# Optimization experiments

Measured on AMD Instinct MI355X. Metric: run time of the kernel, lower is better.

Reference implementation:

```python
import jax, jax.numpy as jnp
import numpy as np

N_HEADS = 12


def gconv1x1(x, w, b, groups):
    # x: [B, C, T, S]; w: [O, C//groups] (1x1 kernel squeezed); b: [O]
    B, C, T, S = x.shape
    O, I = w.shape
    xr = x.reshape(B, groups, C // groups, T, S)
    wr = w.reshape(groups, O // groups, I)
    y = jnp.einsum('bgits,goi->bgots', xr, wr).reshape(B, O, T, S)
    return y + b[None, :, None, None]


def setup_inputs() -> dict:
    key = jax.random.key(0)
    ks = jax.random.split(key, 16)
    B, T, E = 2, 512, 768
    H = N_HEADS
    s = 0.02
    inp = {
        'x': jax.random.normal(ks[0], (B, T, E), jnp.float32),
        # fc_q / fc_k / fc_v (torch Linear: y = x @ W.T + b)
        'wq': jax.random.normal(ks[1], (E, E), jnp.float32) * s,
        'bq': jax.random.normal(ks[2], (E,), jnp.float32) * s,
        'wk': jax.random.normal(ks[3], (E, E), jnp.float32) * s,
        'bk': jax.random.normal(ks[4], (E,), jnp.float32) * s,
        'wv': jax.random.normal(ks[5], (E, E), jnp.float32) * s,
        'bv': jax.random.normal(ks[6], (E,), jnp.float32) * s,
        # ConvolutionOp: all 1x1 grouped convs, groups=12
        # conv_inner_subspace_1: in=144 -> out=96  (w: [96, 12])
        'w1': jax.random.normal(ks[7], (8 * H, H), jnp.float32) * s,
        'b1': jax.random.normal(ks[8], (8 * H,), jnp.float32) * s,
        # conv_inner_subspace_2: in=96 -> out=12   (w: [12, 8])
        'w2': jax.random.normal(ks[9], (H, 8), jnp.float32) * s,
        'b2': jax.random.normal(ks[10], (H,), jnp.float32) * s,
        # conv_cross_subspace_1: in=12 -> out=48   (w: [48, 1])
        'w3': jax.random.normal(ks[11], (4 * H, 1), jnp.float32) * s,
        'b3': jax.random.normal(ks[12], (4 * H,), jnp.float32) * s,
        # conv_cross_subspace_2: in=48 -> out=12   (w: [12, 4])
        'w4': jax.random.normal(ks[13], (H, 4), jnp.float32) * s,
        'b4': jax.random.normal(ks[14], (H,), jnp.float32) * s,
    }
    return inp


def reference(x, wq, bq, wk, bk, wv, bv, w1, b1, w2, b2, w3, b3, w4, b4):
    B, T, E = x.shape
    H = N_HEADS
    hd = E // H
    scale = E ** 0.5  # note: sqrt(embed_dim), not sqrt(head_dim)

    def heads(y):  # [B,T,E] -> [H,B,T,hd]
        return y.reshape(B, T, H, hd).transpose(2, 0, 1, 3)

    q = heads(x @ wq.T + bq)
    k = heads(x @ wk.T + bk)
    v = heads(x @ wv.T + bv)

    # all head-pair QK^T: channel index = q_head * H + k_head (matches torch stack order)
    attn = jnp.einsum('qbld,kbtd->qkblt', q, k) / scale          # [H,H,B,T,T]
    attn = attn.transpose(2, 0, 1, 3, 4).reshape(B, H * H, T, T)  # [B,144,T,T]

    # talking-heads style grouped 1x1 conv mixing
    a = jax.nn.relu(gconv1x1(attn, w1, b1, H))   # [B,96,T,T]
    a = gconv1x1(a, w2, b2, H)                    # [B,12,T,T]
    a = jax.nn.relu(gconv1x1(a, w3, b3, H))      # [B,48,T,T]
    a = gconv1x1(a, w4, b4, H)                    # [B,12,T,T]

    # weighted V sum; rearrange 'head b t d -> b t (head d)'
    ctx = jnp.einsum('bhlt,hbtd->blhd', a, v).reshape(B, T, E)
    return ctx
```

## Files before the change

### kernel.cpp

```cpp
#include <hip/hip_runtime.h>

#define DEVINL __device__ __forceinline__

constexpr int E    = 768;
constexpr int TSEQ = 512;
constexpr int NH   = 12;
constexpr int HD   = 64;
constexpr float RSCALE = 0.036084391824351615f;

typedef short bf16x8 __attribute__((ext_vector_type(8)));
typedef float floatx4 __attribute__((ext_vector_type(4)));

DEVINL short f2bf(float x) {
    union { float f; unsigned u; } v; v.f = x;
    unsigned r = v.u + 0x7FFFu + ((v.u >> 16) & 1u);
    return (short)(r >> 16);
}
DEVINL float bf2f(short s) {
    union { unsigned u; float f; } v;
    v.u = ((unsigned)(unsigned short)s) << 16;
    return v.f;
}

__global__ __launch_bounds__(256) void convert_kernel(
    const float* __restrict__ x,  const float* __restrict__ wq,
    const float* __restrict__ wk, const float* __restrict__ wv,
    short* __restrict__ xb, short* __restrict__ wqb,
    short* __restrict__ wkb, short* __restrict__ wvb)
{
    const int g = blockIdx.x * 256 + threadIdx.x;
    const float* src; short* dst; int off;
    if (g < 98304)       { src = x;  dst = xb;  off = g * 8; }
    else if (g < 172032) { src = wq; dst = wqb; off = (g - 98304) * 8; }
    else if (g < 245760) { src = wk; dst = wkb; off = (g - 172032) * 8; }
    else                 { src = wv; dst = wvb; off = (g - 245760) * 8; }
    float4 f0 = *(const float4*)&src[off];
    float4 f1 = *(const float4*)&src[off + 4];
    bf16x8 o;
    o[0] = f2bf(f0.x); o[1] = f2bf(f0.y); o[2] = f2bf(f0.z); o[3] = f2bf(f0.w);
    o[4] = f2bf(f1.x); o[5] = f2bf(f1.y); o[6] = f2bf(f1.z); o[7] = f2bf(f1.w);
    *(bf16x8*)&dst[off] = o;
}

__global__ __launch_bounds__(256) void qkv_mfma(
    const short* __restrict__ xb,
    const short* __restrict__ wqb, const float* __restrict__ bq,
    const short* __restrict__ wkb, const float* __restrict__ bk,
    const short* __restrict__ wvb, const float* __restrict__ bv,
    short* __restrict__ Qo, short* __restrict__ Ko, short* __restrict__ Vo)
{
    const short* W; const float* bias; short* outp;
    if (blockIdx.z == 0)      { W = wqb; bias = bq; outp = Qo; }
    else if (blockIdx.z == 1) { W = wkb; bias = bk; outp = Ko; }
    else                      { W = wvb; bias = bv; outp = Vo; }

    __shared__ short As[64 * 72];
    __shared__ short Bs[64 * 72];

    const int m0   = blockIdx.x * 64;
    const int n0   = blockIdx.y * 64;
    const int tid  = threadIdx.x;
    const int wvi  = tid >> 6;
    const int lane = tid & 63;
    const int col  = lane & 15;
    const int quad = lane >> 4;

    const int r0 = tid >> 3,   kc0 = tid & 7;
    const int r1 = r0 + 32;

    floatx4 acc[4];
    #pragma unroll
    for (int i = 0; i < 4; i++) acc[i] = (floatx4){0.f, 0.f, 0.f, 0.f};

    for (int k0 = 0; k0 < E; k0 += 64) {
        bf16x8 a0 = *(const bf16x8*)&xb[(size_t)(m0 + r0) * E + k0 + kc0 * 8];
        bf16x8 a1 = *(const bf16x8*)&xb[(size_t)(m0 + r1) * E + k0 + kc0 * 8];
        bf16x8 b0 = *(const bf16x8*)&W [(size_t)(n0 + r0) * E + k0 + kc0 * 8];
        bf16x8 b1 = *(const bf16x8*)&W [(size_t)(n0 + r1) * E + k0 + kc0 * 8];
        __syncthreads();
        *(bf16x8*)&As[r0 * 72 + kc0 * 8] = a0;
        *(bf16x8*)&As[r1 * 72 + kc0 * 8] = a1;
        *(bf16x8*)&Bs[r0 * 72 + kc0 * 8] = b0;
        *(bf16x8*)&Bs[r1 * 72 + kc0 * 8] = b1;
        __syncthreads();
        #pragma unroll
        for (int k32 = 0; k32 < 2; k32++) {
            bf16x8 bf = *(const bf16x8*)&Bs[(wvi*16 + col) * 72 + k32*32 + quad*8];
            #pragma unroll
            for (int ms = 0; ms < 4; ms++) {
                bf16x8 af = *(const bf16x8*)&As[(ms*16 + col) * 72 + k32*32 + quad*8];
                acc[ms] = __builtin_amdgcn_mfma_f32_16x16x32_bf16(af, bf, acc[ms], 0, 0, 0);
            }
        }
    }

    const float bn = bias[n0 + wvi*16 + col];
    const int h = blockIdx.y;
    #pragma unroll
    for (int ms = 0; ms < 4; ms++) {
        #pragma unroll
        for (int r = 0; r < 4; r++) {
            int m = m0 + ms*16 + quad*4 + r;
            int bb = m >> 9, l = m & 511;
            outp[(((size_t)(bb*NH + h)) * TSEQ + l) * HD + wvi*16 + col] =
                f2bf(acc[ms][r] + bn);
        }
    }
}

__global__ __launch_bounds__(256) void kmix_kernel(
    const short* __restrict__ K,
    const float* __restrict__ w1,
    short* __restrict__ Kp)
{
    const int g  = blockIdx.x * 256 + threadIdx.x;
    const int d8 = g & 7;
    const int t  = (g >> 3) & 511;
    const int o  = (g >> 12) & 7;
    const int bh = g >> 15;
    const int h  = bh % NH;
    const int b  = bh / NH;

    float acc[8] = {};
    #pragma unroll
    for (int i = 0; i < 12; i++) {
        float w = w1[(h*8 + o)*12 + i] * RSCALE;
        bf16x8 kv = *(const bf16x8*)&K[(((size_t)(b*NH + i) * TSEQ) + t) * HD + d8*8];
        #pragma unroll
        for (int j = 0; j < 8; j++)
            acc[j] = fmaf(w, bf2f(kv[j]), acc[j]);
    }
    bf16x8 outv;
    #pragma unroll
    for (int j = 0; j < 8; j++) outv[j] = f2bf(acc[j]);
    *(bf16x8*)&Kp[(size_t)g * 8] = outv;
}

DEVINL float mlp_eval(const float s[8],
                      const float b1r[8], const float w2r[8], float b2r,
                      const float w3r[4], const float b3r[4],
                      const float w4r[4], float b4r)
{
    float z2 = b2r;
    #pragma unroll
    for (int o = 0; o < 8; o++) {
        float z1 = fmaxf(s[o] + b1r[o], 0.0f);
        z2 = fmaf(z1, w2r[o], z2);
    }
    float r = b4r;
    #pragma unroll
    for (int j = 0; j < 4; j++) {
        float z3 = fmaxf(fmaf(z2, w3r[j], b3r[j]), 0.0f);
        r = fmaf(z3, w4r[j], r);
    }
    return r;
}

DEVINL int vrow(int r) { return r*40 + (r >> 3)*8; }

__global__ __launch_bounds__(256, 3) void attn_mfma(
    const short* __restrict__ Qg,
    const short* __restrict__ Kg,
    const short* __restrict__ Vg,
    const float* __restrict__ b1, const float* __restrict__ w2,
    const float* __restrict__ b2, const float* __restrict__ w3,
    const float* __restrict__ b3, const float* __restrict__ w4,
    const float* __restrict__ b4,
    float* __restrict__ Pout)
{
    __shared__ short Ks[256 * 72];
    __shared__ short Vt[2624];
    __shared__ short As[2624];

    const int blk = blockIdx.x;
    const int qtr = blk & 3;
    const int lt  = (blk >> 2) & 7;
    const int bh  = blk >> 5;
    const int h   = bh % NH;
    const int l0  = lt * 64;
    const int tb  = qtr * 128;

    const int tid  = threadIdx.x;
    const int wv   = tid >> 6;
    const int lane = tid & 63;
    const int col  = lane & 15;
    const int quad = lane >> 4;
    const int wl   = wv >> 1;
    const int wt   = wv & 1;

    float b1r[8], w2r[8], w3r[4], b3r[4], w4r[4];
    #pragma unroll
    for (int o = 0; o < 8; o++) { b1r[o] = b1[h*8+o]; w2r[o] = w2[h*8+o]; }
    #pragma unroll
    for (int j = 0; j < 4; j++) { w3r[j] = w3[h*4+j]; b3r[j] = b3[h*4+j]; w4r[j] = w4[h*4+j]; }
    const float b2r = b2[h];
    const float b4r = b4[h];

    bf16x8 qa[2][2];
    {
        const short* qb = Qg + ((size_t)bh * TSEQ + l0 + wl*32 + col) * HD;
        qa[0][0] = *(const bf16x8*)&qb[quad*8];
        qa[0][1] = *(const bf16x8*)&qb[32 + quad*8];
        qa[1][0] = *(const bf16x8*)&qb[16*HD + quad*8];
        qa[1][1] = *(const bf16x8*)&qb[16*HD + 32 + quad*8];
    }

    floatx4 accO[4];
    #pragma unroll
    for (int d16 = 0; d16 < 4; d16++) accO[d16] = (floatx4){0.f, 0.f, 0.f, 0.f};

    const short* kbase = Kg + (size_t)bh * 8 * TSEQ * HD;
    const short* vbase = Vg + (size_t)bh * TSEQ * HD;

    const int tl = tid >> 3;
    const int dc = tid & 7;

    for (int it = 0; it < 4; it++) {
        const int t0 = tb + it * 32;

        bf16x8 ktmp[8];
        #pragma unroll
        for (int o = 0; o < 8; o++)
            ktmp[o] = *(const bf16x8*)&kbase[((size_t)o * TSEQ + t0 + tl) * HD + dc*8];
        bf16x8 vtmp = *(const bf16x8*)&vbase[(size_t)(t0 + tl) * HD + dc*8];

        __syncthreads();

        #pragma unroll
        for (int o = 0; o < 8; o++)
            *(bf16x8*)&Ks[(o*32 + tl)*72 + dc*8] = ktmp[o];
        #pragma unroll
        for (int j = 0; j < 8; j++)
            Vt[vrow(dc*8 + j) + tl] = vtmp[j];

        __syncthreads();

        floatx4 accS[8][2];
        #pragma unroll
        for (int o = 0; o < 8; o++) {
            accS[o][0] = (floatx4){0.f, 0.f, 0.f, 0.f};
            accS[o][1] = (floatx4){0.f, 0.f, 0.f, 0.f};
        }
        #pragma unroll
        for (int k32 = 0; k32 < 2; k32++) {
            #pragma unroll
            for (int o = 0; o < 8; o++) {
                bf16x8 bf = *(const bf16x8*)&Ks[(o*32 + wt*16 + col)*72 + k32*32 + quad*8];
                accS[o][0] = __builtin_amdgcn_mfma_f32_16x16x32_bf16(qa[0][k32], bf, accS[o][0], 0, 0, 0);
                accS[o][1] = __builtin_amdgcn_mfma_f32_16x16x32_bf16(qa[1][k32], bf, accS[o][1], 0, 0, 0);
            }
        }

        #pragma unroll
        for (int li = 0; li < 2; li++) {
            #pragma unroll
            for (int r = 0; r < 4; r++) {
                float s[8];
                #pragma unroll
                for (int o = 0; o < 8; o++) s[o] = accS[o][li][r];
                float a = mlp_eval(s, b1r, w2r, b2r, w3r, b3r, w4r, b4r);
                As[vrow(wl*32 + li*16 + quad*4 + r) + wt*16 + col] = f2bf(a);
            }
        }
        __syncthreads();

        bf16x8 af = *(const bf16x8*)&As[vrow(wv*16 + col) + quad*8];
        #pragma unroll
        for (int d16 = 0; d16 < 4; d16++) {
            bf16x8 vf = *(const bf16x8*)&Vt[vrow(d16*16 + col) + quad*8];
            accO[d16] = __builtin_amdgcn_mfma_f32_16x16x32_bf16(af, vf, accO[d16], 0, 0, 0);
        }
    }

    float* pb = Pout + (size_t)blk * 64 * 64;
    #pragma unroll
    for (int d16 = 0; d16 < 4; d16++)
        #pragma unroll
        for (int r = 0; r < 4; r++)
            pb[(wv*16 + quad*4 + r) * 64 + d16*16 + col] = accO[d16][r];
}

__global__ __launch_bounds__(256) void reduce_kernel(
    const float* __restrict__ P, float* __restrict__ out)
{
    const int gi  = blockIdx.x * 256 + threadIdx.x;
    const int d4  = gi & 15;
    const int r   = (gi >> 4) & 63;
    const int grp = gi >> 10;
    const int lt  = grp & 7;
    const int bh  = grp >> 3;
    const int h   = bh % NH;
    const int b   = bh / NH;

    const float* p0 = P + (size_t)grp * 4 * 4096 + r * 64 + d4 * 4;
    float4 s0 = *(const float4*)&p0[0];
    float4 s1 = *(const float4*)&p0[4096];
    float4 s2 = *(const float4*)&p0[8192];
    float4 s3 = *(const float4*)&p0[12288];
    float4 s;
    s.x = (s0.x + s1.x) + (s2.x + s3.x);
    s.y = (s0.y + s1.y) + (s2.y + s3.y);
    s.z = (s0.z + s1.z) + (s2.z + s3.z);
    s.w = (s0.w + s1.w) + (s2.w + s3.w);
    *(float4*)&out[((size_t)(b*TSEQ + lt*64 + r)) * E + h*64 + d4*4] = s;
}

extern "C" void kernel_launch(void* const* d_in, const int* in_sizes, int n_in,
                              void* d_out, int out_size, void* d_ws, size_t ws_size,
                              hipStream_t stream) {
    const float* x  = (const float*)d_in[0];
    const float* wq = (const float*)d_in[1];
    const float* bq = (const float*)d_in[2];
    const float* wk = (const float*)d_in[3];
    const float* bk = (const float*)d_in[4];
    const float* wv = (const float*)d_in[5];
    const float* bv = (const float*)d_in[6];
    const float* w1 = (const float*)d_in[7];
    const float* b1 = (const float*)d_in[8];
    const float* w2 = (const float*)d_in[9];
    const float* b2 = (const float*)d_in[10];
    const float* w3 = (const float*)d_in[11];
    const float* b3 = (const float*)d_in[12];
    const float* w4 = (const float*)d_in[13];
    const float* b4 = (const float*)d_in[14];
    float* out = (float*)d_out;

    short* Qb = (short*)d_ws;
    short* Kb = Qb + 786432;
    short* Vb = Kb + 786432;
    short* Kp = Vb + 786432;
    float* P  = (float*)(Kp + 6291456);
    short* xb  = (short*)P;
    short* wqb = xb + 786432;
    short* wkb = wqb + 589824;
    short* wvb = wkb + 589824;

    convert_kernel<<<1248, 256, 0, stream>>>(x, wq, wk, wv, xb, wqb, wkb, wvb);
    qkv_mfma<<<dim3(16, 12, 3), 256, 0, stream>>>(xb, wqb, bq, wkb, bk, wvb, bv, Qb, Kb, Vb);
    kmix_kernel<<<3072, 256, 0, stream>>>(Kb, w1, Kp);
    attn_mfma<<<768, 256, 0, stream>>>(Qb, Kp, Vb, b1, w2, b2, w3, b3, w4, b4, P);
    reduce_kernel<<<768, 256, 0, stream>>>(P, out);
}
```

Measured before the change: 130.3 us.

## Fuse fp32-to-bf16 conversion into QKV GEMM and double-buffer loads in GEMM and attention

Drops the separate convert kernel: the QKV GEMM now reads fp32 x and weights directly and converts them to bf16 while staging into LDS, using register double buffering so global loads overlap compute. kmix now gives each thread all 8 outputs, so the 12 K heads are loaded once per thread instead of 8 times, and it launches 8x fewer blocks. The attention loop prefetches the next K/V tile into registers, splits the score MFMAs into two halves of 4 channels to reduce live accumulators, and raises wave priority around MFMA sections. In exchange the GEMM moves twice the global bytes (fp32), and the larger register footprint may reduce occupancy.

```diff
diff --git a/kernel.cpp b/kernel.cpp
--- a/kernel.cpp
+++ b/kernel.cpp
@@ -22,37 +22,17 @@
     return v.f;
 }
 
-__global__ __launch_bounds__(256) void convert_kernel(
-    const float* __restrict__ x,  const float* __restrict__ wq,
-    const float* __restrict__ wk, const float* __restrict__ wv,
-    short* __restrict__ xb, short* __restrict__ wqb,
-    short* __restrict__ wkb, short* __restrict__ wvb)
-{
-    const int g = blockIdx.x * 256 + threadIdx.x;
-    const float* src; short* dst; int off;
-    if (g < 98304)       { src = x;  dst = xb;  off = g * 8; }
-    else if (g < 172032) { src = wq; dst = wqb; off = (g - 98304) * 8; }
-    else if (g < 245760) { src = wk; dst = wkb; off = (g - 172032) * 8; }
-    else                 { src = wv; dst = wvb; off = (g - 245760) * 8; }
-    float4 f0 = *(const float4*)&src[off];
-    float4 f1 = *(const float4*)&src[off + 4];
-    bf16x8 o;
-    o[0] = f2bf(f0.x); o[1] = f2bf(f0.y); o[2] = f2bf(f0.z); o[3] = f2bf(f0.w);
-    o[4] = f2bf(f1.x); o[5] = f2bf(f1.y); o[6] = f2bf(f1.z); o[7] = f2bf(f1.w);
-    *(bf16x8*)&dst[off] = o;
-}
-
 __global__ __launch_bounds__(256) void qkv_mfma(
-    const short* __restrict__ xb,
-    const short* __restrict__ wqb, const float* __restrict__ bq,
-    const short* __restrict__ wkb, const float* __restrict__ bk,
-    const short* __restrict__ wvb, const float* __restrict__ bv,
+    const float* __restrict__ x,
+    const float* __restrict__ wq, const float* __restrict__ bq,
+    const float* __restrict__ wk, const float* __restrict__ bk,
+    const float* __restrict__ wv, const float* __restrict__ bv,
     short* __restrict__ Qo, short* __restrict__ Ko, short* __restrict__ Vo)
 {
-    const short* W; const float* bias; short* outp;
-    if (blockIdx.z == 0)      { W = wqb; bias = bq; outp = Qo; }
-    else if (blockIdx.z == 1) { W = wkb; bias = bk; outp = Ko; }
-    else                      { W = wvb; bias = bv; outp = Vo; }
+    const float* W; const float* bias; short* outp;
+    if (blockIdx.z == 0)      { W = wq; bias = bq; outp = Qo; }
+    else if (blockIdx.z == 1) { W = wk; bias = bk; outp = Ko; }
+    else                      { W = wv; bias = bv; outp = Vo; }
 
     __shared__ short As[64 * 72];
     __shared__ short Bs[64 * 72];
@@ -65,34 +45,71 @@
     const int col  = lane & 15;
     const int quad = lane >> 4;
 
-    const int r0 = tid >> 3,   kc0 = tid & 7;
+    const int r0 = tid >> 3, kc0 = tid & 7;
     const int r1 = r0 + 32;
 
     floatx4 acc[4];
     #pragma unroll
     for (int i = 0; i < 4; i++) acc[i] = (floatx4){0.f, 0.f, 0.f, 0.f};
 
-    for (int k0 = 0; k0 < E; k0 += 64) {
-        bf16x8 a0 = *(const bf16x8*)&xb[(size_t)(m0 + r0) * E + k0 + kc0 * 8];
-        bf16x8 a1 = *(const bf16x8*)&xb[(size_t)(m0 + r1) * E + k0 + kc0 * 8];
-        bf16x8 b0 = *(const bf16x8*)&W [(size_t)(n0 + r0) * E + k0 + kc0 * 8];
-        bf16x8 b1 = *(const bf16x8*)&W [(size_t)(n0 + r1) * E + k0 + kc0 * 8];
-        __syncthreads();
-        *(bf16x8*)&As[r0 * 72 + kc0 * 8] = a0;
-        *(bf16x8*)&As[r1 * 72 + kc0 * 8] = a1;
-        *(bf16x8*)&Bs[r0 * 72 + kc0 * 8] = b0;
-        *(bf16x8*)&Bs[r1 * 72 + kc0 * 8] = b1;
-        __syncthreads();
-        #pragma unroll
-        for (int k32 = 0; k32 < 2; k32++) {
-            bf16x8 bf = *(const bf16x8*)&Bs[(wvi*16 + col) * 72 + k32*32 + quad*8];
-            #pragma unroll
-            for (int ms = 0; ms < 4; ms++) {
-                bf16x8 af = *(const bf16x8*)&As[(ms*16 + col) * 72 + k32*32 + quad*8];
-                acc[ms] = __builtin_amdgcn_mfma_f32_16x16x32_bf16(af, bf, acc[ms], 0, 0, 0);
-            }
-        }
-    }
+    float4 st[2][8];
+
+    #define QKV_LOAD(buf, kk) do { \
+        st[buf][0] = *(const float4*)&x[(size_t)(m0 + r0) * E + (kk) + kc0*8]; \
+        st[buf][1] = *(const float4*)&x[(size_t)(m0 + r0) * E + (kk) + kc0*8 + 4]; \
+        st[buf][2] = *(const float4*)&x[(size_t)(m0 + r1) * E + (kk) + kc0*8]; \
+        st[buf][3] = *(const float4*)&x[(size_t)(m0 + r1) * E + (kk) + kc0*8 + 4]; \
+        st[buf][4] = *(const float4*)&W[(size_t)(n0 + r0) * E + (kk) + kc0*8]; \
+        st[buf][5] = *(const float4*)&W[(size_t)(n0 + r0) * E + (kk) + kc0*8 + 4]; \
+        st[buf][6] = *(const float4*)&W[(size_t)(n0 + r1) * E + (kk) + kc0*8]; \
+        st[buf][7] = *(const float4*)&W[(size_t)(n0 + r1) * E + (kk) + kc0*8 + 4]; \
+    } while (0)
+
+    #define QKV_STORE(dst, lo, hi) do { \
+        bf16x8 o_; \
+        o_[0] = f2bf((lo).x); o_[1] = f2bf((lo).y); o_[2] = f2bf((lo).z); o_[3] = f2bf((lo).w); \
+        o_[4] = f2bf((hi).x); o_[5] = f2bf((hi).y); o_[6] = f2bf((hi).z); o_[7] = f2bf((hi).w); \
+        *(bf16x8*)(dst) = o_; \
+    } while (0)
+
+    #define QKV_STAGE(buf) do { \
+        QKV_STORE(&As[r0*72 + kc0*8], st[buf][0], st[buf][1]); \
+        QKV_STORE(&As[r1*72 + kc0*8], st[buf][2], st[buf][3]); \
+        QKV_STORE(&Bs[r0*72 + kc0*8], st[buf][4], st[buf][5]); \
+        QKV_STORE(&Bs[r1*72 + kc0*8], st[buf][6], st[buf][7]); \
+    } while (0)
+
+    #define QKV_COMPUTE() do { \
+        _Pragma("unroll") \
+        for (int k32 = 0; k32 < 2; ++k32) { \
+            bf16x8 bfr = *(const bf16x8*)&Bs[(wvi*16 + col)*72 + k32*32 + quad*8]; \
+            _Pragma("unroll") \
+            for (int ms = 0; ms < 4; ++ms) { \
+                bf16x8 afr = *(const bf16x8*)&As[(ms*16 + col)*72 + k32*32 + quad*8]; \
+                acc[ms] = __builtin_amdgcn_mfma_f32_16x16x32_bf16(afr, bfr, acc[ms], 0, 0, 0); \
+            } \
+        } \
+    } while (0)
+
+    QKV_LOAD(0, 0);
+    #pragma unroll 1
+    for (int it2 = 0; it2 < 6; ++it2) {
+        const int k0 = it2 * 128;
+        __syncthreads();
+        QKV_STAGE(0);
+        QKV_LOAD(1, k0 + 64);
+        __syncthreads();
+        QKV_COMPUTE();
+        __syncthreads();
+        QKV_STAGE(1);
+        if (it2 < 5) QKV_LOAD(0, k0 + 128);
+        __syncthreads();
+        QKV_COMPUTE();
+    }
+    #undef QKV_LOAD
+    #undef QKV_STORE
+    #undef QKV_STAGE
+    #undef QKV_COMPUTE
 
     const float bn = bias[n0 + wvi*16 + col];
     const int h = blockIdx.y;
@@ -116,44 +133,33 @@
     const int g  = blockIdx.x * 256 + threadIdx.x;
     const int d8 = g & 7;
     const int t  = (g >> 3) & 511;
-    const int o  = (g >> 12) & 7;
-    const int bh = g >> 15;
+    const int bh = g >> 12;
     const int h  = bh % NH;
     const int b  = bh / NH;
 
-    float acc[8] = {};
-    #pragma unroll
-    for (int i = 0; i < 12; i++) {
-        float w = w1[(h*8 + o)*12 + i] * RSCALE;
-        bf16x8 kv = *(const bf16x8*)&K[(((size_t)(b*NH + i) * TSEQ) + t) * HD + d8*8];
-        #pragma unroll
-        for (int j = 0; j < 8; j++)
-            acc[j] = fmaf(w, bf2f(kv[j]), acc[j]);
-    }
-    bf16x8 outv;
-    #pragma unroll
-    for (int j = 0; j < 8; j++) outv[j] = f2bf(acc[j]);
-    *(bf16x8*)&Kp[(size_t)g * 8] = outv;
-}
-
-DEVINL float mlp_eval(const float s[8],
-                      const float b1r[8], const float w2r[8], float b2r,
-                      const float w3r[4], const float b3r[4],
-                      const float w4r[4], float b4r)
-{
-    float z2 = b2r;
-    #pragma unroll
-    for (int o = 0; o < 8; o++) {
-        float z1 = fmaxf(s[o] + b1r[o], 0.0f);
-        z2 = fmaf(z1, w2r[o], z2);
-    }
-    float r = b4r;
-    #pragma unroll
-    for (int j = 0; j < 4; j++) {
-        float z3 = fmaxf(fmaf(z2, w3r[j], b3r[j]), 0.0f);
-        r = fmaf(z3, w4r[j], r);
-    }
-    return r;
+    float kv[12][8];
+    #pragma unroll
+    for (int i = 0; i < 12; ++i) {
+        bf16x8 raw = *(const bf16x8*)&K[(((size_t)(b*NH + i)) * TSEQ + t) * HD + d8*8];
+        #pragma unroll
+        for (int j = 0; j < 8; ++j) kv[i][j] = bf2f(raw[j]);
+    }
+
+    short* outbase = Kp + (((size_t)bh * 8) * TSEQ + t) * HD + d8*8;
+    #pragma unroll
+    for (int o = 0; o < 8; ++o) {
+        float acc[8] = {};
+        #pragma unroll
+        for (int i = 0; i < 12; ++i) {
+            const float w = w1[(h*8 + o)*12 + i] * RSCALE;
+            #pragma unroll
+            for (int j = 0; j < 8; ++j) acc[j] = fmaf(w, kv[i][j], acc[j]);
+        }
+        bf16x8 ov;
+        #pragma unroll
+        for (int j = 0; j < 8; ++j) ov[j] = f2bf(acc[j]);
+        *(bf16x8*)&outbase[(size_t)o * TSEQ * HD] = ov;
+    }
 }
 
 DEVINL int vrow(int r) { return r*40 + (r >> 3)*8; }
@@ -215,62 +221,106 @@
     const int tl = tid >> 3;
     const int dc = tid & 7;
 
-    for (int it = 0; it < 4; it++) {
-        const int t0 = tb + it * 32;
-
-        bf16x8 ktmp[8];
-        #pragma unroll
-        for (int o = 0; o < 8; o++)
-            ktmp[o] = *(const bf16x8*)&kbase[((size_t)o * TSEQ + t0 + tl) * HD + dc*8];
-        bf16x8 vtmp = *(const bf16x8*)&vbase[(size_t)(t0 + tl) * HD + dc*8];
-
-        __syncthreads();
-
-        #pragma unroll
-        for (int o = 0; o < 8; o++)
-            *(bf16x8*)&Ks[(o*32 + tl)*72 + dc*8] = ktmp[o];
-        #pragma unroll
-        for (int j = 0; j < 8; j++)
-            Vt[vrow(dc*8 + j) + tl] = vtmp[j];
-
-        __syncthreads();
-
-        floatx4 accS[8][2];
-        #pragma unroll
-        for (int o = 0; o < 8; o++) {
-            accS[o][0] = (floatx4){0.f, 0.f, 0.f, 0.f};
-            accS[o][1] = (floatx4){0.f, 0.f, 0.f, 0.f};
-        }
-        #pragma unroll
-        for (int k32 = 0; k32 < 2; k32++) {
-            #pragma unroll
-            for (int o = 0; o < 8; o++) {
-                bf16x8 bf = *(const bf16x8*)&Ks[(o*32 + wt*16 + col)*72 + k32*32 + quad*8];
-                accS[o][0] = __builtin_amdgcn_mfma_f32_16x16x32_bf16(qa[0][k32], bf, accS[o][0], 0, 0, 0);
-                accS[o][1] = __builtin_amdgcn_mfma_f32_16x16x32_bf16(qa[1][k32], bf, accS[o][1], 0, 0, 0);
-            }
-        }
-
-        #pragma unroll
-        for (int li = 0; li < 2; li++) {
-            #pragma unroll
-            for (int r = 0; r < 4; r++) {
-                float s[8];
-                #pragma unroll
-                for (int o = 0; o < 8; o++) s[o] = accS[o][li][r];
-                float a = mlp_eval(s, b1r, w2r, b2r, w3r, b3r, w4r, b4r);
-                As[vrow(wl*32 + li*16 + quad*4 + r) + wt*16 + col] = f2bf(a);
-            }
-        }
-        __syncthreads();
-
-        bf16x8 af = *(const bf16x8*)&As[vrow(wv*16 + col) + quad*8];
-        #pragma unroll
-        for (int d16 = 0; d16 < 4; d16++) {
-            bf16x8 vf = *(const bf16x8*)&Vt[vrow(d16*16 + col) + quad*8];
-            accO[d16] = __builtin_amdgcn_mfma_f32_16x16x32_bf16(af, vf, accO[d16], 0, 0, 0);
-        }
-    }
+    bf16x8 kt[2][8];
+    bf16x8 vt2[2];
+
+    #define ATTN_LOAD(buf, t0) do { \
+        _Pragma("unroll") \
+        for (int o_ = 0; o_ < 8; ++o_) \
+            kt[buf][o_] = *(const bf16x8*)&kbase[((size_t)o_ * TSEQ + (t0) + tl) * HD + dc*8]; \
+        vt2[buf] = *(const bf16x8*)&vbase[(size_t)((t0) + tl) * HD + dc*8]; \
+    } while (0)
+
+    #define ATTN_STAGE(buf) do { \
+        _Pragma("unroll") \
+        for (int o_ = 0; o_ < 8; ++o_) \
+            *(bf16x8*)&Ks[(o_*32 + tl)*72 + dc*8] = kt[buf][o_]; \
+        _Pragma("unroll") \
+        for (int j_ = 0; j_ < 8; ++j_) \
+            Vt[vrow(dc*8 + j_) + tl] = vt2[buf][j_]; \
+    } while (0)
+
+    #define ATTN_COMPUTE() do { \
+        float z2a[8]; \
+        _Pragma("unroll") \
+        for (int i_ = 0; i_ < 8; ++i_) z2a[i_] = b2r; \
+        _Pragma("unroll") \
+        for (int oh = 0; oh < 2; ++oh) { \
+            floatx4 accS[4][2]; \
+            _Pragma("unroll") \
+            for (int o4 = 0; o4 < 4; ++o4) { \
+                accS[o4][0] = (floatx4){0.f, 0.f, 0.f, 0.f}; \
+                accS[o4][1] = (floatx4){0.f, 0.f, 0.f, 0.f}; \
+            } \
+            __builtin_amdgcn_s_setprio(1); \
+            _Pragma("unroll") \
+            for (int k32 = 0; k32 < 2; ++k32) { \
+                _Pragma("unroll") \
+                for (int o4 = 0; o4 < 4; ++o4) { \
+                    const int o_ = oh*4 + o4; \
+                    bf16x8 bfr = *(const bf16x8*)&Ks[(o_*32 + wt*16 + col)*72 + k32*32 + quad*8]; \
+                    accS[o4][0] = __builtin_amdgcn_mfma_f32_16x16x32_bf16(qa[0][k32], bfr, accS[o4][0], 0, 0, 0); \
+                    accS[o4][1] = __builtin_amdgcn_mfma_f32_16x16x32_bf16(qa[1][k32], bfr, accS[o4][1], 0, 0, 0); \
+                } \
+            } \
+            __builtin_amdgcn_s_setprio(0); \
+            _Pragma("unroll") \
+            for (int li = 0; li < 2; ++li) { \
+                _Pragma("unroll") \
+                for (int r = 0; r < 4; ++r) { \
+                    _Pragma("unroll") \
+                    for (int o4 = 0; o4 < 4; ++o4) { \
+                        float z1 = fmaxf(accS[o4][li][r] + b1r[oh*4+o4], 0.0f); \
+                        z2a[li*4+r] = fmaf(z1, w2r[oh*4+o4], z2a[li*4+r]); \
+                    } \
+                } \
+            } \
+        } \
+        _Pragma("unroll") \
+        for (int li = 0; li < 2; ++li) { \
+            _Pragma("unroll") \
+            for (int r = 0; r < 4; ++r) { \
+                float z2 = z2a[li*4+r]; \
+                float a_ = b4r; \
+                _Pragma("unroll") \
+                for (int j_ = 0; j_ < 4; ++j_) { \
+                    float z3 = fmaxf(fmaf(z2, w3r[j_], b3r[j_]), 0.0f); \
+                    a_ = fmaf(z3, w4r[j_], a_); \
+                } \
+                As[vrow(wl*32 + li*16 + quad*4 + r) + wt*16 + col] = f2bf(a_); \
+            } \
+        } \
+        __syncthreads(); \
+        { \
+            bf16x8 afr = *(const bf16x8*)&As[vrow(wv*16 + col) + quad*8]; \
+            __builtin_amdgcn_s_setprio(1); \
+            _Pragma("unroll") \
+            for (int d16 = 0; d16 < 4; ++d16) { \
+                bf16x8 vfr = *(const bf16x8*)&Vt[vrow(d16*16 + col) + quad*8]; \
+                accO[d16] = __builtin_amdgcn_mfma_f32_16x16x32_bf16(afr, vfr, accO[d16], 0, 0, 0); \
+            } \
+            __builtin_amdgcn_s_setprio(0); \
+        } \
+    } while (0)
+
+    ATTN_LOAD(0, tb);
+    #pragma unroll 1
+    for (int it2 = 0; it2 < 2; ++it2) {
+        const int t0 = tb + it2 * 64;
+        __syncthreads();
+        ATTN_STAGE(0);
+        ATTN_LOAD(1, t0 + 32);
+        __syncthreads();
+        ATTN_COMPUTE();
+        __syncthreads();
+        ATTN_STAGE(1);
+        if (it2 == 0) ATTN_LOAD(0, t0 + 64);
+        __syncthreads();
+        ATTN_COMPUTE();
+    }
+    #undef ATTN_LOAD
+    #undef ATTN_STAGE
+    #undef ATTN_COMPUTE
 
     float* pb = Pout + (size_t)blk * 64 * 64;
     #pragma unroll
@@ -330,14 +380,9 @@
     short* Vb = Kb + 786432;
     short* Kp = Vb + 786432;
     float* P  = (float*)(Kp + 6291456);
-    short* xb  = (short*)P;
-    short* wqb = xb + 786432;
-    short* wkb = wqb + 589824;
-    short* wvb = wkb + 589824;
-
-    convert_kernel<<<1248, 256, 0, stream>>>(x, wq, wk, wv, xb, wqb, wkb, wvb);
-    qkv_mfma<<<dim3(16, 12, 3), 256, 0, stream>>>(xb, wqb, bq, wkb, bk, wvb, bv, Qb, Kb, Vb);
-    kmix_kernel<<<3072, 256, 0, stream>>>(Kb, w1, Kp);
+
+    qkv_mfma<<<dim3(16, 12, 3), 256, 0, stream>>>(x, wq, bq, wk, bk, wv, bv, Qb, Kb, Vb);
+    kmix_kernel<<<384, 256, 0, stream>>>(Kb, w1, Kp);
     attn_mfma<<<768, 256, 0, stream>>>(Qb, Kp, Vb, b1, w2, b2, w3, b3, w4, b4, P);
     reduce_kernel<<<768, 256, 0, stream>>>(P, out);
 }
```

Result: slower. 137.1 us (+5.2%).
